# Performance work log

Measured on AMD Instinct MI355X. Metric: run time of the kernel, lower is better.

## Reference

```python
import jax, jax.numpy as jnp
import numpy as np

N_LAYERS = 4
D_MODEL = 1024
D_INNER = 2048
DT_RANK = 64
D_STATE = 16
D_CONV = 4
EPS = 1e-5


def _rms(x, w):
    return x * jax.lax.rsqrt(jnp.mean(x * x, axis=-1, keepdims=True) + EPS) * w


def _silu(x):
    return x * jax.nn.sigmoid(x)


def setup_inputs() -> dict:
    key = jax.random.key(0)
    ks = jax.random.split(key, 8)
    B, L = 2, 1024
    s = 0.02
    nl, dm, di = N_LAYERS, D_MODEL, D_INNER
    return {
        "x": jax.random.normal(ks[0], (B, L, dm), dtype=jnp.float32),
        "norm_w": jnp.ones((nl, dm), dtype=jnp.float32),
        "W_in": jax.random.normal(ks[1], (nl, 2 * di, dm), dtype=jnp.float32) * s,
        "conv_w": jax.random.normal(ks[2], (nl, di, D_CONV), dtype=jnp.float32) * s,
        "conv_b": jnp.zeros((nl, di), dtype=jnp.float32),
        "W_x": jax.random.normal(ks[3], (nl, DT_RANK + 2 * D_STATE, di), dtype=jnp.float32) * s,
        "W_dt": jax.random.normal(ks[4], (nl, di, DT_RANK), dtype=jnp.float32) * (DT_RANK ** -0.5),
        "b_dt": jax.random.normal(ks[5], (nl, di), dtype=jnp.float32) - 3.0,  # softplus -> small dt, like inv-softplus init
        "A_log": jax.random.uniform(ks[6], (nl, di, D_STATE), dtype=jnp.float32) * 2.0,  # A = -exp(A_log) in [-7.4, -1]
        "D": jnp.ones((nl, di), dtype=jnp.float32),
        "W_out": jax.random.normal(ks[7], (nl, dm, di), dtype=jnp.float32) * s,
    }


def reference(x, norm_w, W_in, conv_w, conv_b, W_x, W_dt, b_dt, A_log, D, W_out):
    nl = W_in.shape[0]
    L = x.shape[1]
    dc = conv_w.shape[-1]
    n = A_log.shape[-1]
    rk = W_dt.shape[-1]

    def combine(left, right):
        a1, b1 = left
        a2, b2 = right
        return a2 * a1, a2 * b1 + b2

    for i in range(nl):
        h = _rms(x, norm_w[i])
        xz = jnp.einsum('bld,ed->ble', h, W_in[i])          # [B,L,2*Di]
        xi, z = jnp.split(xz, 2, axis=-1)
        # causal depthwise conv1d (padding=dc-1, keep first L outputs)
        xp = jnp.pad(xi, ((0, 0), (dc - 1, 0), (0, 0)))
        xc = conv_b[i] + sum(xp[:, k:k + L, :] * conv_w[i][:, k] for k in range(dc))
        xc = _silu(xc)
        # SSM parameterization
        dbc = jnp.einsum('bld,ed->ble', xc, W_x[i])          # [B,L,rk+2n]
        delta, Bm, Cm = jnp.split(dbc, [rk, rk + n], axis=-1)
        delta = jax.nn.softplus(jnp.einsum('blr,dr->bld', delta, W_dt[i]) + b_dt[i])  # [B,L,Di]
        A = -jnp.exp(A_log[i])                               # [Di,N]
        deltaA = jnp.exp(delta[..., None] * A)               # [B,L,Di,N]
        BX = (delta * xc)[..., None] * Bm[:, :, None, :]     # [B,L,Di,N]
        # parallel scan: h_t = deltaA_t * h_{t-1} + BX_t
        _, hs = jax.lax.associative_scan(combine, (deltaA, BX), axis=1)
        y = jnp.einsum('bldn,bln->bld', hs, Cm) + D[i] * xc
        out = jnp.einsum('bld,ed->ble', y * _silu(z), W_out[i])
        x = x + out
    return x
```

## Files before the change

kernel.cpp:

```cpp
#include <hip/hip_runtime.h>
#include <hip/hip_bf16.h>
#include <math.h>

#define NL 4
#define DM 1024
#define DI 2048
#define RK 64
#define NS 16
#define LSEQ 1024
#define BATCH 2
#define MROWS (BATCH*LSEQ)
#define NCHUNK 32
#define LC 32

typedef __attribute__((ext_vector_type(8))) short bf16x8;
typedef __attribute__((ext_vector_type(4))) float f32x4;

__device__ __forceinline__ float bf2f(unsigned short u){
  union { unsigned int i; float f; } v; v.i = ((unsigned int)u) << 16; return v.f;
}
__device__ __forceinline__ unsigned short f2bf(float f){
  union { float f; unsigned int i; } v; v.f = f;
  unsigned int r = v.i + 0x7fffu + ((v.i >> 16) & 1u);
  return (unsigned short)(r >> 16);
}
__device__ __forceinline__ float sigmoidf_(float x){ return 1.0f / (1.0f + __expf(-x)); }

__device__ __forceinline__ void gl2lds16(const void* g, void* l) {
  __builtin_amdgcn_global_load_lds((__attribute__((address_space(1))) void*)g,
                                   (__attribute__((address_space(3))) void*)l,
                                   16, 0, 0);
}

template<int BM, int BN, int WAVES_M, int WAVES_N, int EPI>
__global__ __launch_bounds__(256)
void gemm_bt(const unsigned short* __restrict__ A, const unsigned short* __restrict__ W,
             void* __restrict__ C, int M, int N, int K, int ldc, int kslices)
{
  constexpr int MT = BM / (WAVES_M * 16);
  constexpr int NT = BN / (WAVES_N * 16);
  __shared__ __align__(16) unsigned short As[BM * 64];
  __shared__ __align__(16) unsigned short Bs[BN * 64];

  const int tid  = threadIdx.x;
  const int wave = tid >> 6;
  const int lane = tid & 63;
  const int wm   = wave / WAVES_N;
  const int wn   = wave % WAVES_N;
  const int quad = lane >> 4;
  const int l16  = lane & 15;
  const int srow = lane >> 3;
  const int scol = ((lane & 7) ^ srow) * 8;

  const int m0 = blockIdx.x * BM;
  const int n0 = blockIdx.y * BN;
  const int Ks = K / kslices;
  const int kb = blockIdx.z * Ks;

  f32x4 acc[MT][NT];
  #pragma unroll
  for (int i = 0; i < MT; i++)
    #pragma unroll
    for (int j = 0; j < NT; j++)
      acc[i][j] = (f32x4){0.f, 0.f, 0.f, 0.f};

  for (int k0 = kb; k0 < kb + Ks; k0 += 64) {
    const unsigned short* Ab = A + (size_t)m0 * K + k0;
    #pragma unroll
    for (int i = 0; i < BM / 32; i++) {
      int c = i * 4 + wave;
      gl2lds16(Ab + (size_t)(c * 8 + srow) * K + scol, As + c * 512);
    }
    const unsigned short* Wb = W + (size_t)n0 * K + k0;
    #pragma unroll
    for (int i = 0; i < BN / 32; i++) {
      int c = i * 4 + wave;
      gl2lds16(Wb + (size_t)(c * 8 + srow) * K + scol, Bs + c * 512);
    }
    __syncthreads();

    #pragma unroll
    for (int h = 0; h < 2; h++) {
      bf16x8 af[MT], bfr[NT];
      #pragma unroll
      for (int mt = 0; mt < MT; mt++) {
        int rA = wm * MT * 16 + mt * 16 + l16;
        af[mt] = *(const bf16x8*)(As + rA * 64 + (((h * 4 + quad) ^ (rA & 7)) << 3));
      }
      #pragma unroll
      for (int nt = 0; nt < NT; nt++) {
        int rB = wn * NT * 16 + nt * 16 + l16;
        bfr[nt] = *(const bf16x8*)(Bs + rB * 64 + (((h * 4 + quad) ^ (rB & 7)) << 3));
      }
      #pragma unroll
      for (int mt = 0; mt < MT; mt++)
        #pragma unroll
        for (int nt = 0; nt < NT; nt++)
          acc[mt][nt] = __builtin_amdgcn_mfma_f32_16x16x32_bf16(af[mt], bfr[nt], acc[mt][nt], 0, 0, 0);
    }
    __syncthreads();
  }

  const size_t slice_off = (size_t)blockIdx.z * M * ldc;
  #pragma unroll
  for (int mt = 0; mt < MT; mt++) {
    #pragma unroll
    for (int nt = 0; nt < NT; nt++) {
      int n = n0 + wn * NT * 16 + nt * 16 + l16;
      #pragma unroll
      for (int r = 0; r < 4; r++) {
        int m = m0 + wm * MT * 16 + mt * 16 + quad * 4 + r;
        float v = acc[mt][nt][r];
        size_t off = (size_t)m * ldc + n;
        if constexpr (EPI == 0)      ((unsigned short*)C)[off] = f2bf(v);
        else                         ((float*)C)[slice_off + off] = v;
      }
    }
  }
}

#define G3R 8
#define G3C 256
#define G3P 264
__global__ __launch_bounds__(256)
void gemm3_fused(const float* __restrict__ dbc, const unsigned short* __restrict__ Wdt,
                 const float* __restrict__ b_dt, unsigned short* __restrict__ delta)
{
  __shared__ float dts[G3R][RK];
  __shared__ __align__(16) unsigned short Ws[RK][G3P];
  const int tid = threadIdx.x;
  const int m0 = blockIdx.x * G3R;
  const int c0 = blockIdx.y * G3C;

  {
    int r = tid >> 5, k = (tid & 31) * 2;
    float2 v = *(const float2*)(dbc + (size_t)(m0 + r) * 96 + k);
    dts[r][k] = v.x; dts[r][k + 1] = v.y;
  }
  {
    const unsigned short* wrow = Wdt + (size_t)(c0 + tid) * RK;
    #pragma unroll
    for (int ch = 0; ch < 8; ch++) {
      union { bf16x8 v; unsigned short u[8]; } w;
      w.v = *(const bf16x8*)(wrow + ch * 8);
      #pragma unroll
      for (int j = 0; j < 8; j++) Ws[ch * 8 + j][tid] = w.u[j];
    }
  }
  __syncthreads();

  const int r  = tid >> 5;
  const int cg = tid & 31;
  float acc[8] = {0.f, 0.f, 0.f, 0.f, 0.f, 0.f, 0.f, 0.f};
  #pragma unroll 4
  for (int k = 0; k < RK; k++) {
    float a = dts[r][k];
    union { bf16x8 v; unsigned short u[8]; } w;
    w.v = *(const bf16x8*)&Ws[k][cg * 8];
    #pragma unroll
    for (int j = 0; j < 8; j++) acc[j] += a * bf2f(w.u[j]);
  }

  const int m = m0 + r, c = c0 + cg * 8;
  float4 b0 = *(const float4*)(b_dt + c);
  float4 b1 = *(const float4*)(b_dt + c + 4);
  float bb[8] = {b0.x, b0.y, b0.z, b0.w, b1.x, b1.y, b1.z, b1.w};
  union { unsigned short u[8]; uint4 v; } o;
  #pragma unroll
  for (int j = 0; j < 8; j++) {
    float v = acc[j] + bb[j];
    o.u[j] = f2bf((v > 15.0f) ? v : __logf(1.0f + __expf(v)));
  }
  *(uint4*)(delta + (size_t)m * DI + c) = o.v;
}

__global__ __launch_bounds__(256)
void reduce4_kernel(const float* __restrict__ part, float* __restrict__ x)
{
  const size_t MN = (size_t)MROWS * DM;
  int i = blockIdx.x * 256 + threadIdx.x;
  float4 a = ((const float4*)part)[i];
  float4 b = ((const float4*)(part + MN))[i];
  float4 o = ((float4*)x)[i];
  o.x += a.x + b.x;
  o.y += a.y + b.y;
  o.z += a.z + b.z;
  o.w += a.w + b.w;
  ((float4*)x)[i] = o;
}

__global__ __launch_bounds__(256)
void reduce2_kernel(const float* __restrict__ part, float* __restrict__ dbc)
{
  const int MN = MROWS * 96;
  int i = blockIdx.x * 256 + threadIdx.x;
  dbc[i] = part[i] + part[MN + i] + part[2 * MN + i] + part[3 * MN + i];
}

__global__ __launch_bounds__(256)
void rmsnorm_kernel(const float* __restrict__ x, const float* __restrict__ w,
                    unsigned short* __restrict__ h)
{
  const int row = blockIdx.x;
  const float4 a = ((const float4*)(x + (size_t)row * DM))[threadIdx.x];
  float ss = a.x*a.x + a.y*a.y + a.z*a.z + a.w*a.w;
  #pragma unroll
  for (int o = 32; o > 0; o >>= 1) ss += __shfl_down(ss, o);
  __shared__ float red[4];
  if ((threadIdx.x & 63) == 0) red[threadIdx.x >> 6] = ss;
  __syncthreads();
  float rs = rsqrtf((red[0] + red[1] + red[2] + red[3]) * (1.0f / DM) + 1e-5f);
  const float4 wv = ((const float4*)w)[threadIdx.x];
  ushort4 o4;
  o4.x = f2bf(a.x * rs * wv.x);
  o4.y = f2bf(a.y * rs * wv.y);
  o4.z = f2bf(a.z * rs * wv.z);
  o4.w = f2bf(a.w * rs * wv.w);
  ((ushort4*)(h + (size_t)row * DM))[threadIdx.x] = o4;
}

__global__ __launch_bounds__(256)
void conv_silu_kernel(const unsigned short* __restrict__ xz,
                      const float* __restrict__ cw, const float* __restrict__ cb,
                      unsigned short* __restrict__ xc)
{
  int idx = blockIdx.x * 256 + threadIdx.x;
  int d = idx & (DI - 1);
  int t = (idx >> 11) & (LSEQ - 1);
  int b = idx >> 21;
  const float4 w4 = ((const float4*)cw)[d];
  const float wk[4] = {w4.x, w4.y, w4.z, w4.w};
  const unsigned short* xi = xz + (size_t)b * LSEQ * (2 * DI) + d;
  float acc = cb[d];
  #pragma unroll
  for (int k = 0; k < 4; k++) {
    int tt = t - 3 + k;
    if (tt >= 0) acc += bf2f(xi[(size_t)tt * (2 * DI)]) * wk[k];
  }
  xc[idx] = f2bf(acc * sigmoidf_(acc));
}

#define SEG0 (NL*2*DI*DM)
#define SEG1 (SEG0 + NL*96*DI)
#define SEG2 (SEG1 + NL*DI*RK)
#define SEG3 (SEG2 + NL*DM*DI)
__global__ void convert_all_kernel(const float* __restrict__ W_in, unsigned short* __restrict__ Win_bf,
                                   const float* __restrict__ W_x,  unsigned short* __restrict__ Wx_bf,
                                   const float* __restrict__ W_dt, unsigned short* __restrict__ Wdt_bf,
                                   const float* __restrict__ W_out,unsigned short* __restrict__ Wout_bf)
{
  const int T8 = SEG3 / 8;
  int stride = gridDim.x * 256;
  for (int i = blockIdx.x * 256 + threadIdx.x; i < T8; i += stride) {
    int e = i * 8;
    const float* s; unsigned short* d; int off;
    if (e < SEG0)      { s = W_in;  d = Win_bf;  off = e; }
    else if (e < SEG1) { s = W_x;   d = Wx_bf;   off = e - SEG0; }
    else if (e < SEG2) { s = W_dt;  d = Wdt_bf;  off = e - SEG1; }
    else               { s = W_out; d = Wout_bf; off = e - SEG2; }
    float4 a = *(const float4*)(s + off);
    float4 b = *(const float4*)(s + off + 4);
    union { unsigned short u[8]; uint4 v; } o;
    o.u[0] = f2bf(a.x); o.u[1] = f2bf(a.y); o.u[2] = f2bf(a.z); o.u[3] = f2bf(a.w);
    o.u[4] = f2bf(b.x); o.u[5] = f2bf(b.y); o.u[6] = f2bf(b.z); o.u[7] = f2bf(b.w);
    *(uint4*)(d + off) = o.v;
  }
}

__global__ __launch_bounds__(256)
void scan1_kernel(const unsigned short* __restrict__ delta, const unsigned short* __restrict__ xc,
                  const float* __restrict__ dbc, const float* __restrict__ A_log,
                  float* __restrict__ hend, float* __restrict__ sumd)
{
  const int d = blockIdx.x * 256 + threadIdx.x;
  const int c = blockIdx.y;
  const int b = blockIdx.z;
  const int t0 = c * LC;
  __shared__ float bc[LC][32];
  #pragma unroll
  for (int i = 0; i < (LC * 32) / 256; i++) {
    int f = i * 256 + threadIdx.x;
    int r = f >> 5, col = f & 31;
    bc[r][col] = dbc[(size_t)(b * LSEQ + t0 + r) * 96 + 64 + col];
  }
  float Av[NS], h[NS];
  #pragma unroll
  for (int n = 0; n < NS; n++) { Av[n] = -__expf(A_log[(size_t)d * NS + n]); h[n] = 0.f; }
  __syncthreads();
  float sd = 0.f;
  for (int t = 0; t < LC; t++) {
    size_t ix = (size_t)(b * LSEQ + t0 + t) * DI + d;
    float dt = bf2f(delta[ix]);
    float xcv = bf2f(xc[ix]);
    sd += dt;
    float dx = dt * xcv;
    #pragma unroll
    for (int n = 0; n < NS; n++) {
      float da = __expf(dt * Av[n]);
      h[n] = da * h[n] + dx * bc[t][n];
    }
  }
  size_t base = ((size_t)(b * NCHUNK + c) * NS) * DI + d;
  #pragma unroll
  for (int n = 0; n < NS; n++) hend[base + (size_t)n * DI] = h[n];
  sumd[(size_t)(b * NCHUNK + c) * DI + d] = sd;
}

__global__ __launch_bounds__(256)
void scan2_kernel(const float* __restrict__ A_log, const float* __restrict__ hend,
                  const float* __restrict__ sumd, float* __restrict__ hin)
{
  int g = blockIdx.x * 256 + threadIdx.x;
  int b = g >> 11;
  int d = g & (DI - 1);
  float Av[NS], H[NS];
  #pragma unroll
  for (int n = 0; n < NS; n++) { Av[n] = -__expf(A_log[(size_t)d * NS + n]); H[n] = 0.f; }
  for (int c = 0; c < NCHUNK; c++) {
    size_t base = ((size_t)(b * NCHUNK + c) * NS) * DI + d;
    float sd = sumd[(size_t)(b * NCHUNK + c) * DI + d];
    #pragma unroll
    for (int n = 0; n < NS; n++) {
      hin[base + (size_t)n * DI] = H[n];
      float da = __expf(Av[n] * sd);
      H[n] = da * H[n] + hend[base + (size_t)n * DI];
    }
  }
}

__global__ __launch_bounds__(256)
void scan3_kernel(const unsigned short* __restrict__ delta, const unsigned short* __restrict__ xc,
                  const float* __restrict__ dbc, const float* __restrict__ A_log,
                  const float* __restrict__ hin, const float* __restrict__ Dvec,
                  const unsigned short* __restrict__ xz, unsigned short* __restrict__ g)
{
  const int d = blockIdx.x * 256 + threadIdx.x;
  const int c = blockIdx.y;
  const int b = blockIdx.z;
  const int t0 = c * LC;
  __shared__ float bc[LC][32];
  #pragma unroll
  for (int i = 0; i < (LC * 32) / 256; i++) {
    int f = i * 256 + threadIdx.x;
    int r = f >> 5, col = f & 31;
    bc[r][col] = dbc[(size_t)(b * LSEQ + t0 + r) * 96 + 64 + col];
  }
  float Av[NS], h[NS];
  size_t base = ((size_t)(b * NCHUNK + c) * NS) * DI + d;
  #pragma unroll
  for (int n = 0; n < NS; n++) {
    Av[n] = -__expf(A_log[(size_t)d * NS + n]);
    h[n] = hin[base + (size_t)n * DI];
  }
  const float Dd = Dvec[d];
  __syncthreads();
  for (int t = 0; t < LC; t++) {
    size_t ix = (size_t)(b * LSEQ + t0 + t) * DI + d;
    float dt = bf2f(delta[ix]);
    float xcv = bf2f(xc[ix]);
    float dx = dt * xcv;
    float y = Dd * xcv;
    #pragma unroll
    for (int n = 0; n < NS; n++) {
      float da = __expf(dt * Av[n]);
      h[n] = da * h[n] + dx * bc[t][n];
      y += h[n] * bc[t][16 + n];
    }
    float zv = bf2f(xz[(size_t)(b * LSEQ + t0 + t) * (2 * DI) + DI + d]);
    g[ix] = f2bf(y * (zv * sigmoidf_(zv)));
  }
}

extern "C" void kernel_launch(void* const* d_in, const int* in_sizes, int n_in,
                              void* d_out, int out_size, void* d_ws, size_t ws_size,
                              hipStream_t stream)
{
  const float* x_in   = (const float*)d_in[0];
  const float* norm_w = (const float*)d_in[1];
  const float* W_in   = (const float*)d_in[2];
  const float* conv_w = (const float*)d_in[3];
  const float* conv_b = (const float*)d_in[4];
  const float* W_x    = (const float*)d_in[5];
  const float* W_dt   = (const float*)d_in[6];
  const float* b_dt   = (const float*)d_in[7];
  const float* A_log  = (const float*)d_in[8];
  const float* Dv     = (const float*)d_in[9];
  const float* W_out  = (const float*)d_in[10];
  float* x = (float*)d_out;

  char* p = (char*)d_ws;
  auto alloc = [&](size_t bytes) {
    void* r = (void*)p;
    p += (bytes + 255) & ~(size_t)255;
    return r;
  };
  unsigned short* Win_bf  = (unsigned short*)alloc((size_t)NL * 2 * DI * DM * 2);
  unsigned short* Wx_bf   = (unsigned short*)alloc((size_t)NL * 96 * DI * 2);
  unsigned short* Wdt_bf  = (unsigned short*)alloc((size_t)NL * DI * RK * 2);
  unsigned short* Wout_bf = (unsigned short*)alloc((size_t)NL * DM * DI * 2);
  unsigned short* h_bf    = (unsigned short*)alloc((size_t)MROWS * DM * 2);
  unsigned short* xz_bf   = (unsigned short*)alloc((size_t)MROWS * 2 * DI * 2);
  unsigned short* xc_bf   = (unsigned short*)alloc((size_t)MROWS * DI * 2);
  float*          dbc     = (float*)alloc((size_t)MROWS * 96 * 4);
  unsigned short* g_bf    = (unsigned short*)alloc((size_t)MROWS * DI * 2);
  unsigned short* delta   = (unsigned short*)alloc((size_t)MROWS * DI * 2);
  float*          hend    = (float*)alloc((size_t)BATCH * NCHUNK * NS * DI * 4);
  float*          hin     = (float*)alloc((size_t)BATCH * NCHUNK * NS * DI * 4);
  float*          sumd    = (float*)alloc((size_t)BATCH * NCHUNK * DI * 4);
  float* part2 = hend;
  float* part4 = hend;

  hipMemcpyAsync(x, x_in, (size_t)MROWS * DM * 4, hipMemcpyDeviceToDevice, stream);

  convert_all_kernel<<<2048, 256, 0, stream>>>(W_in, Win_bf, W_x, Wx_bf,
                                               W_dt, Wdt_bf, W_out, Wout_bf);

  for (int l = 0; l < NL; l++) {
    const unsigned short* Win_l  = Win_bf  + (size_t)l * 2 * DI * DM;
    const unsigned short* Wx_l   = Wx_bf   + (size_t)l * 96 * DI;
    const unsigned short* Wdt_l  = Wdt_bf  + (size_t)l * DI * RK;
    const unsigned short* Wout_l = Wout_bf + (size_t)l * DM * DI;

    rmsnorm_kernel<<<MROWS, 256, 0, stream>>>(x, norm_w + (size_t)l * DM, h_bf);

    gemm_bt<64, 128, 2, 2, 0><<<dim3(MROWS / 64, (2 * DI) / 128), 256, 0, stream>>>(
        h_bf, Win_l, xz_bf, MROWS, 2 * DI, DM, 2 * DI, 1);

    conv_silu_kernel<<<(BATCH * LSEQ * DI) / 256, 256, 0, stream>>>(
        xz_bf, conv_w + (size_t)l * DI * 4, conv_b + (size_t)l * DI, xc_bf);

    gemm_bt<64, 96, 4, 1, 4><<<dim3(MROWS / 64, 1, 4), 256, 0, stream>>>(
        xc_bf, Wx_l, part2, MROWS, 96, DI, 96, 4);
    reduce2_kernel<<<(MROWS * 96) / 256, 256, 0, stream>>>(part2, dbc);

    gemm3_fused<<<dim3(MROWS / G3R, DI / G3C), 256, 0, stream>>>(
        dbc, Wdt_l, b_dt + (size_t)l * DI, delta);

    scan1_kernel<<<dim3(DI / 256, NCHUNK, BATCH), 256, 0, stream>>>(
        delta, xc_bf, dbc, A_log + (size_t)l * DI * NS, hend, sumd);
    scan2_kernel<<<(BATCH * DI) / 256, 256, 0, stream>>>(
        A_log + (size_t)l * DI * NS, hend, sumd, hin);
    scan3_kernel<<<dim3(DI / 256, NCHUNK, BATCH), 256, 0, stream>>>(
        delta, xc_bf, dbc, A_log + (size_t)l * DI * NS, hin, Dv + (size_t)l * DI, xz_bf, g_bf);

    gemm_bt<64, 128, 2, 2, 4><<<dim3(MROWS / 64, DM / 128, 2), 256, 0, stream>>>(
        g_bf, Wout_l, part4, MROWS, DM, DI, DM, 2);
    reduce4_kernel<<<(MROWS * DM) / 1024, 256, 0, stream>>>(part4, x);
  }
}
```

Baseline: 844.4 us.

## Replace split-K partial buffers and reduce kernels with atomic accumulation

The split-K GEMMs for the x-projection and output projection now atomically add their partial results straight into the destination (dbc after a memset, and the residual x) instead of writing per-slice partial buffers and running separate reduce kernels. This removes two kernel launches per layer and the extra round trip of partial sums through memory. The cost is float atomics in the epilogue, with nondeterministic summation order and possible contention. The weight conversion kernel also switches to nontemporal loads and stores and launches twice as many blocks.

```diff
diff --git a/kernel.cpp b/kernel.cpp
--- a/kernel.cpp
+++ b/kernel.cpp
@@ -15,6 +15,7 @@
 
 typedef __attribute__((ext_vector_type(8))) short bf16x8;
 typedef __attribute__((ext_vector_type(4))) float f32x4;
+typedef __attribute__((ext_vector_type(4))) unsigned int u32x4;
 
 __device__ __forceinline__ float bf2f(unsigned short u){
   union { unsigned int i; float f; } v; v.i = ((unsigned int)u) << 16; return v.f;
@@ -101,7 +102,6 @@
     __syncthreads();
   }
 
-  const size_t slice_off = (size_t)blockIdx.z * M * ldc;
   #pragma unroll
   for (int mt = 0; mt < MT; mt++) {
     #pragma unroll
@@ -113,7 +113,7 @@
         float v = acc[mt][nt][r];
         size_t off = (size_t)m * ldc + n;
         if constexpr (EPI == 0)      ((unsigned short*)C)[off] = f2bf(v);
-        else                         ((float*)C)[slice_off + off] = v;
+        else                         atomicAdd((float*)C + off, v);
       }
     }
   }
@@ -165,36 +165,13 @@
   float4 b0 = *(const float4*)(b_dt + c);
   float4 b1 = *(const float4*)(b_dt + c + 4);
   float bb[8] = {b0.x, b0.y, b0.z, b0.w, b1.x, b1.y, b1.z, b1.w};
-  union { unsigned short u[8]; uint4 v; } o;
+  union { unsigned short u[8]; u32x4 v; } o;
   #pragma unroll
   for (int j = 0; j < 8; j++) {
     float v = acc[j] + bb[j];
     o.u[j] = f2bf((v > 15.0f) ? v : __logf(1.0f + __expf(v)));
   }
-  *(uint4*)(delta + (size_t)m * DI + c) = o.v;
-}
-
-__global__ __launch_bounds__(256)
-void reduce4_kernel(const float* __restrict__ part, float* __restrict__ x)
-{
-  const size_t MN = (size_t)MROWS * DM;
-  int i = blockIdx.x * 256 + threadIdx.x;
-  float4 a = ((const float4*)part)[i];
-  float4 b = ((const float4*)(part + MN))[i];
-  float4 o = ((float4*)x)[i];
-  o.x += a.x + b.x;
-  o.y += a.y + b.y;
-  o.z += a.z + b.z;
-  o.w += a.w + b.w;
-  ((float4*)x)[i] = o;
-}
-
-__global__ __launch_bounds__(256)
-void reduce2_kernel(const float* __restrict__ part, float* __restrict__ dbc)
-{
-  const int MN = MROWS * 96;
-  int i = blockIdx.x * 256 + threadIdx.x;
-  dbc[i] = part[i] + part[MN + i] + part[2 * MN + i] + part[3 * MN + i];
+  *(u32x4*)(delta + (size_t)m * DI + c) = o.v;
 }
 
 __global__ __launch_bounds__(256)
@@ -258,12 +235,12 @@
     else if (e < SEG1) { s = W_x;   d = Wx_bf;   off = e - SEG0; }
     else if (e < SEG2) { s = W_dt;  d = Wdt_bf;  off = e - SEG1; }
     else               { s = W_out; d = Wout_bf; off = e - SEG2; }
-    float4 a = *(const float4*)(s + off);
-    float4 b = *(const float4*)(s + off + 4);
-    union { unsigned short u[8]; uint4 v; } o;
+    f32x4 a = __builtin_nontemporal_load((const f32x4*)(s + off));
+    f32x4 b = __builtin_nontemporal_load((const f32x4*)(s + off + 4));
+    union { unsigned short u[8]; u32x4 v; } o;
     o.u[0] = f2bf(a.x); o.u[1] = f2bf(a.y); o.u[2] = f2bf(a.z); o.u[3] = f2bf(a.w);
     o.u[4] = f2bf(b.x); o.u[5] = f2bf(b.y); o.u[6] = f2bf(b.z); o.u[7] = f2bf(b.w);
-    *(uint4*)(d + off) = o.v;
+    __builtin_nontemporal_store(o.v, (u32x4*)(d + off));
   }
 }
 
@@ -407,12 +384,10 @@
   float*          hend    = (float*)alloc((size_t)BATCH * NCHUNK * NS * DI * 4);
   float*          hin     = (float*)alloc((size_t)BATCH * NCHUNK * NS * DI * 4);
   float*          sumd    = (float*)alloc((size_t)BATCH * NCHUNK * DI * 4);
-  float* part2 = hend;
-  float* part4 = hend;
 
   hipMemcpyAsync(x, x_in, (size_t)MROWS * DM * 4, hipMemcpyDeviceToDevice, stream);
 
-  convert_all_kernel<<<2048, 256, 0, stream>>>(W_in, Win_bf, W_x, Wx_bf,
+  convert_all_kernel<<<4096, 256, 0, stream>>>(W_in, Win_bf, W_x, Wx_bf,
                                                W_dt, Wdt_bf, W_out, Wout_bf);
 
   for (int l = 0; l < NL; l++) {
@@ -429,9 +404,9 @@
     conv_silu_kernel<<<(BATCH * LSEQ * DI) / 256, 256, 0, stream>>>(
         xz_bf, conv_w + (size_t)l * DI * 4, conv_b + (size_t)l * DI, xc_bf);
 
-    gemm_bt<64, 96, 4, 1, 4><<<dim3(MROWS / 64, 1, 4), 256, 0, stream>>>(
-        xc_bf, Wx_l, part2, MROWS, 96, DI, 96, 4);
-    reduce2_kernel<<<(MROWS * 96) / 256, 256, 0, stream>>>(part2, dbc);
+    hipMemsetAsync(dbc, 0, (size_t)MROWS * 96 * 4, stream);
+    gemm_bt<64, 96, 4, 1, 1><<<dim3(MROWS / 64, 1, 4), 256, 0, stream>>>(
+        xc_bf, Wx_l, dbc, MROWS, 96, DI, 96, 4);
 
     gemm3_fused<<<dim3(MROWS / G3R, DI / G3C), 256, 0, stream>>>(
         dbc, Wdt_l, b_dt + (size_t)l * DI, delta);
@@ -443,8 +418,7 @@
     scan3_kernel<<<dim3(DI / 256, NCHUNK, BATCH), 256, 0, stream>>>(
         delta, xc_bf, dbc, A_log + (size_t)l * DI * NS, hin, Dv + (size_t)l * DI, xz_bf, g_bf);
 
-    gemm_bt<64, 128, 2, 2, 4><<<dim3(MROWS / 64, DM / 128, 2), 256, 0, stream>>>(
-        g_bf, Wout_l, part4, MROWS, DM, DI, DM, 2);
-    reduce4_kernel<<<(MROWS * DM) / 1024, 256, 0, stream>>>(part4, x);
-  }
-}
+    gemm_bt<64, 128, 2, 2, 1><<<dim3(MROWS / 64, DM / 128, 2), 256, 0, stream>>>(
+        g_bf, Wout_l, x, MROWS, DM, DI, DM, 2);
+  }
+}
```

New measurement: 897.8 us. 6.3% more time.
